# Kernel optimization log

Measured on AMD Instinct MI355X. Metric: run time of the kernel, lower is better.

Reference implementation:

```python
import jax, jax.numpy as jnp
import numpy as np
import math

B, C_LOW, C_HIGH, H, W = 8, 128, 256, 128, 128
KS = 7

def _conv(x, w, b, pad):
    out = jax.lax.conv_general_dilated(
        x, w, window_strides=(1, 1), padding=[(pad, pad), (pad, pad)],
        dimension_numbers=('NCHW', 'OIHW', 'NCHW'))
    return out + b[None, :, None, None]

def setup_inputs() -> dict:
    key = jax.random.key(0)
    ks = jax.random.split(key, 6)
    def he(k, shape):  # matches torch init: normal(0, sqrt(2/(kh*kw*out)))
        n = shape[2] * shape[3] * shape[0]
        return jax.random.normal(k, shape, jnp.float32) * math.sqrt(2.0 / n)
    return {
        'cur_low': jax.random.normal(ks[0], (B, C_LOW, H, W), jnp.float32),
        'key_low': jax.random.normal(ks[1], (B, C_LOW, H, W), jnp.float32),
        'key_high': jax.random.normal(ks[2], (B, C_HIGH, H, W), jnp.float32),
        'w_red': he(ks[3], (256, C_LOW, 3, 3)),
        'b_red': jnp.zeros((256,), jnp.float32),
        'w2': he(ks[4], (256, 512, 3, 3)),
        'b2': jnp.zeros((256,), jnp.float32),
        'w3': he(ks[5], (KS * KS, 256, 1, 1)),
        'b3': jnp.zeros((KS * KS,), jnp.float32),
    }

def reference(cur_low, key_low, key_high, w_red, b_red, w2, b2, w3, b3):
    # KernelWeightPredictor
    cur = jax.nn.relu(_conv(cur_low, w_red, b_red, 1))
    key = jax.nn.relu(_conv(key_low, w_red, b_red, 1))
    x = jax.nn.relu(_conv(jnp.concatenate([cur, key], axis=1), w2, b2, 1))
    x = jax.nn.relu(_conv(x, w3, b3, 0))            # [B, k*k, H, W]
    x = jax.nn.softmax(x, axis=1)
    b, k2, h, w = x.shape
    kernels = jnp.transpose(x, (0, 2, 3, 1)).reshape(b, h, w, KS, KS)
    # SpatiallyVariantConvolution: per-pixel 7x7 kernel applied to key_high
    pad = KS // 2
    fp = jnp.pad(key_high, ((0, 0), (0, 0), (pad, pad), (pad, pad)))
    out = jnp.zeros_like(key_high)
    for i in range(KS):          # fixed 49-iteration unrolled loop; avoids
        for j in range(KS):      # materializing the [B,C,H,W,K,K] patch tensor
            out = out + fp[:, :, i:i + h, j:j + w] * kernels[:, None, :, :, i, j]
    return out
```

## Files before the change

### kernel.cpp

```cpp
#include <hip/hip_runtime.h>
#include <stdint.h>
#include <stddef.h>

#define BN   8
#define HN   128
#define WN   128
#define HP   130
#define CLOW 128
#define CMID 256
#define KO   49

#define KHB_H 134
#define KHB_W 144
#define KHB_PLANE (KHB_H * KHB_W)

typedef __attribute__((ext_vector_type(4))) float f32x4;
typedef __attribute__((ext_vector_type(8))) short bf16x8;

typedef __attribute__((address_space(1))) const uint8_t ga_u8;
typedef __attribute__((address_space(3))) uint8_t lds_u8;

__device__ __forceinline__ short f2bf(float f) {
    uint32_t u = __float_as_uint(f);
    u += 0x7fffu + ((u >> 16) & 1u);
    return (short)(u >> 16);
}
__device__ __forceinline__ float bf2f(short s) {
    return __uint_as_float(((uint32_t)(uint16_t)s) << 16);
}
__device__ __forceinline__ void gload16(const void* g, void* l) {
    __builtin_amdgcn_global_load_lds((ga_u8*)g, (lds_u8*)l, 16, 0, 0);
}

__global__ __launch_bounds__(256) void zero_border_all_kernel(
    short* __restrict__ b0, short* __restrict__ b1,
    short* __restrict__ b2, short* __restrict__ b3) {
    const int which = blockIdx.y;
    short* buf = (which == 0) ? b0 : (which == 1) ? b1 : (which == 2) ? b2 : b3;
    const int gsh = (which < 2) ? 4 : 5;
    const int C = (which < 2) ? 128 : 256;
    int t = blockIdx.x * 256 + threadIdx.x;
    int cell = t >> gsh, g = t & ((1 << gsh) - 1);
    if (cell >= 8 * 516) return;
    int b = cell / 516, r = cell - b * 516;
    int y, x;
    if (r < 260) { y = (r >= 130) ? 129 : 0; x = (r >= 130) ? (r - 130) : r; }
    else { int j = r - 260; y = 1 + (j >> 1); x = (j & 1) ? 129 : 0; }
    uint4 z = {0u, 0u, 0u, 0u};
    *(uint4*)&buf[(((size_t)b * HP + y) * HP + x) * C + g * 8] = z;
}

__global__ __launch_bounds__(256) void convert_pad_kernel(
    const float* __restrict__ src0, const float* __restrict__ src1,
    short* __restrict__ dst0, short* __restrict__ dst1) {
    __shared__ short t[128 * 136];
    const int tid = threadIdx.x;
    const int by = blockIdx.x;
    const int b = by >> 7, y = by & 127;
    const float* src = blockIdx.y ? src1 : src0;
    short* dst = blockIdx.y ? dst1 : dst0;
    #pragma unroll
    for (int k = 0; k < 16; ++k) {
        int slot = k * 256 + tid;
        int c = slot >> 5, xg = slot & 31;
        f32x4 v = *(const f32x4*)&src[(((size_t)b * CLOW + c) * HN + y) * WN + xg * 4];
        #pragma unroll
        for (int j = 0; j < 4; ++j) t[(xg * 4 + j) * 136 + c] = f2bf(v[j]);
    }
    __syncthreads();
    short* drow = dst + (((size_t)b * HP + (y + 1)) * HP + 1) * CLOW;
    #pragma unroll
    for (int k = 0; k < 8; ++k) {
        int slot = k * 256 + tid;
        int x = slot >> 4, cg = slot & 15;
        *(bf16x8*)&drow[x * CLOW + cg * 8] = *(const bf16x8*)&t[x * 136 + cg * 8];
    }
}

__global__ __launch_bounds__(256) void pack_w_all_kernel(
    const float* __restrict__ w1, short* __restrict__ wp1,
    const float* __restrict__ w2, short* __restrict__ wp2,
    const float* __restrict__ w3, short* __restrict__ wp3) {
    int i = blockIdx.x * 256 + threadIdx.x;
    if (i < 256 * 1152 + 256 * 4608) {
        const float* w; short* wp; int CIN, K;
        if (i < 256 * 1152) { w = w1; wp = wp1; CIN = 128; K = 1152; }
        else { i -= 256 * 1152; w = w2; wp = wp2; CIN = 512; K = 4608; }
        int cout = i / K;
        int r = i - cout * K;
        int t = r >> 6;
        int j = r & 63;
        int cb = t / 9;
        int tap = t - cb * 9;
        int cin = cb * 64 + j;
        wp[i] = f2bf(w[((size_t)cout * CIN + cin) * 9 + tap]);
    } else {
        int j = i - (256 * 1152 + 256 * 4608);
        if (j >= 64 * 256) return;
        int o = j >> 8, ch = j & 255;
        wp3[j] = (o < KO) ? f2bf(w3[o * 256 + ch]) : (short)0;
    }
}

template <int CIN, bool OPAD, bool FUSE>
__global__ __launch_bounds__(512, 2) void conv_8ph_kernel(
    const short* __restrict__ in_a, const short* __restrict__ in_b,
    const short* __restrict__ wp, const float* __restrict__ bias,
    short* __restrict__ out_a, short* __restrict__ out_b,
    const short* __restrict__ w3p, const float* __restrict__ b3,
    float* __restrict__ z) {
    constexpr int K = 9 * CIN;
    constexpr int NT = K / 64;
    constexpr bool DUAL = (CIN == 512);
    constexpr int PST = DUAL ? 256 : CIN;
    extern __shared__ __align__(16) short lds[];
    const int tid = threadIdx.x;
    int bx = blockIdx.x;
    bx = (bx & 7) * 64 + (bx >> 3);
    const int b = bx >> 6, y0 = (bx & 63) << 1;
    const short* inA = DUAL ? in_a : (blockIdx.z ? in_b : in_a);
    const short* inB = DUAL ? in_b : inA;
    short* out = (!DUAL && blockIdx.z) ? out_b : out_a;

    const int lane = tid & 63, wv = tid >> 6;
    const int wm = wv >> 2, wn = wv & 3;
    const int lr = lane & 15, lk = lane >> 4;

    const int rA = tid >> 3, cc = tid & 7;
    const int cs = cc ^ (rA & 7);
    const int pthrA0 = rA * PST + cs * 8;
    const int pthrA1 = (rA + 64) * PST + cs * 8;
    const int pthrB0 = rA * K + cs * 8;
    const int pthrB1 = (rA + 64) * K + cs * 8;
    const int dA0 = rA * 64 + cc * 8;
    const int dB0 = rA * 64 + cc * 8;

    const int arow = (wm * 128 + lr) * 64;
    const int brow = (wn * 64 + lr) * 64;
    const int cof0 = ((lk) ^ (lr & 7)) * 8;
    const int cof1 = ((4 + lk) ^ (lr & 7)) * 8;

    f32x4 acc[8][4];
    f32x4 zero = {0.f, 0.f, 0.f, 0.f};
    #pragma unroll
    for (int i = 0; i < 8; ++i)
        #pragma unroll
        for (int j = 0; j < 4; ++j) acc[i][j] = zero;

    auto STAGE2 = [&](int t2, int which, short* bufA, short* bufB) {
        const int cb = (t2 * 57) >> 9;
        const int tap = t2 - cb * 9;
        const int ch0v = cb << 6;
        const short* src = (!DUAL || ch0v < 256) ? inA : inB;
        const int ch0 = DUAL ? (ch0v & 255) : ch0v;
        const int ky = (tap * 11) >> 5;
        const int kx = tap - ky * 3;
        if (which == 0 || which == 2) {
            const int po = (which == 0) ? pthrA0 : pthrA1;
            const int doff = (which == 0) ? 0 : 64 * 64;
            const short* s0 = src + ((size_t)(b * HP + (y0 + ky)) * HP + kx) * PST + ch0;
            gload16(s0 + po, bufA + doff + dA0);
            gload16(s0 + (HP * PST) + po, bufA + 128 * 64 + doff + dA0);
        } else {
            const int h2 = (which == 1) ? 0 : 1;
            const short* sb = wp + (size_t)(h2 * 128) * K + t2 * 64;
            short* d = bufB + h2 * 128 * 64 + dB0;
            gload16(sb + pthrB0, d);
            gload16(sb + pthrB1, d + 64 * 64);
        }
    };

    auto LDA = [&](const short* bufA, int mh, bf16x8 (&a)[4][2]) {
        #pragma unroll
        for (int i = 0; i < 4; ++i) {
            const int ro = arow + (mh * 64 + i * 16) * 64;
            a[i][0] = *(const bf16x8*)(bufA + ro + cof0);
            a[i][1] = *(const bf16x8*)(bufA + ro + cof1);
        }
    };
    auto LDB = [&](const short* bufB, int nh, bf16x8 (&bb)[2][2]) {
        #pragma unroll
        for (int j = 0; j < 2; ++j) {
            const int ro = brow + (nh * 32 + j * 16) * 64;
            bb[j][0] = *(const bf16x8*)(bufB + ro + cof0);
            bb[j][1] = *(const bf16x8*)(bufB + ro + cof1);
        }
    };

#define MFMA_Q(A_, B_, MH, NH) do { \
    _Pragma("unroll") \
    for (int i_ = 0; i_ < 4; ++i_) { \
        _Pragma("unroll") \
        for (int j_ = 0; j_ < 2; ++j_) { \
            acc[(MH)*4+i_][(NH)*2+j_] = __builtin_amdgcn_mfma_f32_16x16x32_bf16( \
                A_[i_][0], B_[j_][0], acc[(MH)*4+i_][(NH)*2+j_], 0, 0, 0); \
            acc[(MH)*4+i_][(NH)*2+j_] = __builtin_amdgcn_mfma_f32_16x16x32_bf16( \
                A_[i_][1], B_[j_][1], acc[(MH)*4+i_][(NH)*2+j_], 0, 0, 0); \
        } \
    } } while (0)

    short* const A0 = lds;
    short* const A1 = lds + 16384;
    short* const B0 = lds + 32768;
    short* const B1 = lds + 49152;

    STAGE2(0, 0, A0, B0); STAGE2(0, 1, A0, B0);
    STAGE2(0, 2, A0, B0); STAGE2(0, 3, A0, B0);

    auto TILE = [&](int t, short* bufA, short* bufB, short* nA, short* nB) {
        __builtin_amdgcn_s_barrier();
        __builtin_amdgcn_sched_barrier(0);
        const int t1 = t + 1;
        if (t1 < NT) {
            STAGE2(t1, 0, nA, nB); STAGE2(t1, 1, nA, nB);
            STAGE2(t1, 2, nA, nB); STAGE2(t1, 3, nA, nB);
            __builtin_amdgcn_sched_barrier(0);
            asm volatile("s_waitcnt vmcnt(8)" ::: "memory");
        } else {
            __builtin_amdgcn_sched_barrier(0);
            asm volatile("s_waitcnt vmcnt(0)" ::: "memory");
        }
        __builtin_amdgcn_sched_barrier(0);
        __builtin_amdgcn_s_barrier();
        __builtin_amdgcn_sched_barrier(0);
        bf16x8 ar[4][2], br0[2][2], br1[2][2];
        LDA(bufA, 0, ar);
        LDB(bufB, 0, br0);
        LDB(bufB, 1, br1);
        __builtin_amdgcn_s_setprio(1);
        MFMA_Q(ar, br0, 0, 0);
        MFMA_Q(ar, br1, 0, 1);
        __builtin_amdgcn_s_setprio(0);
        LDA(bufA, 1, ar);
        __builtin_amdgcn_s_setprio(1);
        MFMA_Q(ar, br0, 1, 0);
        MFMA_Q(ar, br1, 1, 1);
        __builtin_amdgcn_s_setprio(0);
    };

    for (int t = 0; t < NT; t += 2) {
        TILE(t,     A0, B0, A1, B1);
        TILE(t + 1, A1, B1, A0, B0);
    }
#undef MFMA_Q

    float bvs[4];
    #pragma unroll
    for (int nf = 0; nf < 4; ++nf) bvs[nf] = bias[wn * 64 + nf * 16 + lr];

    if constexpr (!FUSE) {
        #pragma unroll
        for (int mf = 0; mf < 8; ++mf) {
            #pragma unroll
            for (int rr = 0; rr < 4; ++rr) {
                const int p = wm * 128 + mf * 16 + lk * 4 + rr;
                const int y = y0 + (p >> 7), x = p & 127;
                short* op;
                if (OPAD)
                    op = out + ((size_t)(b * HP + (y + 1)) * HP + (x + 1)) * CMID + wn * 64 + lr;
                else
                    op = out + ((size_t)((b * HN + y) * WN + x)) * CMID + wn * 64 + lr;
                #pragma unroll
                for (int nf = 0; nf < 4; ++nf)
                    op[nf * 16] = f2bf(fmaxf(acc[mf][nf][rr] + bvs[nf], 0.f));
            }
        }
    } else {
        __syncthreads();
        short* const Xh  = lds;
        short* const W3s = lds + 32768;

        #pragma unroll
        for (int sweep = 0; sweep < 4; ++sweep) {
            const int s = sweep * 512 + tid;
            const int o = s >> 5, c = s & 31;
            gload16(w3p + o * 256 + ((c ^ (o & 7)) << 3), W3s + s * 8);
        }

        const int oo = wn * 16 + lr;
        const float b3v = (oo < KO) ? b3[oo] : 0.f;

        #pragma unroll 1
        for (int r = 0; r < 2; ++r) {
            if (wm == r) {
                #pragma unroll
                for (int nf = 0; nf < 4; ++nf) {
                    const int ch = wn * 64 + nf * 16 + lr;
                    const int ck = ch >> 3, el = ch & 7;
                    #pragma unroll
                    for (int mf = 0; mf < 8; ++mf) {
                        #pragma unroll
                        for (int rr = 0; rr < 4; ++rr) {
                            const int px = mf * 16 + lk * 4 + rr;
                            Xh[px * 256 + ((ck ^ (px & 7)) << 3) + el] =
                                f2bf(fmaxf(acc[mf][nf][rr] + bvs[nf], 0.f));
                        }
                    }
                }
            }
            __syncthreads();
            f32x4 a2[4];
            #pragma unroll
            for (int m = 0; m < 4; ++m) {
                a2[m][0] = b3v; a2[m][1] = b3v; a2[m][2] = b3v; a2[m][3] = b3v;
            }
            #pragma unroll
            for (int ks = 0; ks < 8; ++ks) {
                const bf16x8 bfr =
                    *(const bf16x8*)&W3s[oo * 256 + (((ks * 4 + lk) ^ (oo & 7)) << 3)];
                #pragma unroll
                for (int m = 0; m < 4; ++m) {
                    const int px = wm * 64 + m * 16 + lr;
                    const bf16x8 afr =
                        *(const bf16x8*)&Xh[px * 256 + (((ks * 4 + lk) ^ (px & 7)) << 3)];
                    a2[m] = __builtin_amdgcn_mfma_f32_16x16x32_bf16(afr, bfr, a2[m], 0, 0, 0);
                }
            }
            float* zp = z + ((size_t)(b * 16384 + (y0 + r) * 128)) * 64;
            #pragma unroll
            for (int m = 0; m < 4; ++m) {
                #pragma unroll
                for (int r2 = 0; r2 < 4; ++r2) {
                    const int px = wm * 64 + m * 16 + lk * 4 + r2;
                    zp[px * 64 + oo] = a2[m][r2];
                }
            }
            if (r == 0) __syncthreads();
        }
    }
}

__global__ __launch_bounds__(256) void pad_kh_kernel(
    const float* __restrict__ kh, short* __restrict__ khb) {
    const int bc = blockIdx.x;
    const float* src = kh + (size_t)bc * (HN * WN);
    short* dst = khb + (size_t)bc * KHB_PLANE;
    for (int i = threadIdx.x; i < KHB_H * (KHB_W / 8); i += 256) {
        int yy = i / (KHB_W / 8);
        int g = i - yy * (KHB_W / 8);
        int ys = yy - 3;
        bf16x8 v;
        #pragma unroll
        for (int t = 0; t < 8; ++t) {
            int xs = g * 8 + t - 4;
            float f = 0.f;
            if ((unsigned)ys < 128u && (unsigned)xs < 128u) f = src[(ys << 7) + xs];
            v[t] = f2bf(f);
        }
        *(bf16x8*)&dst[yy * KHB_W + g * 8] = v;
    }
}

__global__ __launch_bounds__(256) void svc4_kernel(
    const float* __restrict__ z, const short* __restrict__ khb,
    float* __restrict__ out) {
    __shared__ float a_s[KO * 64];
    const int tid = threadIdx.x;
    int by = blockIdx.y;
    by = (by & 7) * 128 + (by >> 3);
    const int b = by >> 7, y = by & 127;
    const int x0 = blockIdx.x * 64;

    {
        const int px = tid >> 2, l = tid & 3;
        const float* zp = z + ((size_t)(b * 16384 + (y << 7) + x0 + px)) * 64 + l * 16;
        float v[16];
        #pragma unroll
        for (int q = 0; q < 4; ++q) {
            f32x4 t4 = *(const f32x4*)&zp[q * 4];
            v[q * 4 + 0] = fmaxf(t4[0], 0.f);
            v[q * 4 + 1] = fmaxf(t4[1], 0.f);
            v[q * 4 + 2] = fmaxf(t4[2], 0.f);
            v[q * 4 + 3] = fmaxf(t4[3], 0.f);
        }
        #pragma unroll
        for (int j = 1; j < 16; ++j) if (l == 3) v[j] = -1e30f;
        float m = v[0];
        #pragma unroll
        for (int j = 1; j < 16; ++j) m = fmaxf(m, v[j]);
        m = fmaxf(m, __shfl_xor(m, 1, 64));
        m = fmaxf(m, __shfl_xor(m, 2, 64));
        float s = 0.f;
        #pragma unroll
        for (int j = 0; j < 16; ++j) { v[j] = __expf(v[j] - m); s += v[j]; }
        s += __shfl_xor(s, 1, 64);
        s += __shfl_xor(s, 2, 64);
        const float inv = 1.f / s;
        #pragma unroll
        for (int j = 0; j < 16; ++j) {
            const int o = l * 16 + j;
            if (o < KO) a_s[o * 64 + px] = v[j] * inv;
        }
    }
    __syncthreads();

    const int ci = tid >> 3;
    const int pg = tid & 7;
    const int p0 = x0 + pg * 8;

    float acc[8][8];
    #pragma unroll
    for (int c = 0; c < 8; ++c)
        #pragma unroll
        for (int j = 0; j < 8; ++j) acc[c][j] = 0.f;

    const short* kbase = khb + (((size_t)b * 256 + ci) * KHB_H + y) * KHB_W + p0;

    #pragma unroll 1
    for (int dy = 0; dy < 7; ++dy) {
        f32x4 av[14];
        #pragma unroll
        for (int dx = 0; dx < 7; ++dx) {
            av[dx * 2]     = *(const f32x4*)&a_s[(dy * 7 + dx) * 64 + pg * 8];
            av[dx * 2 + 1] = *(const f32x4*)&a_s[(dy * 7 + dx) * 64 + pg * 8 + 4];
        }
        const short* krow = kbase + dy * KHB_W;
        #pragma unroll
        for (int c = 0; c < 8; ++c) {
            const short* kp = krow + (size_t)c * 32 * KHB_PLANE;
            bf16x8 k0 = *(const bf16x8*)(kp);
            bf16x8 k1 = *(const bf16x8*)(kp + 8);
            float win[16];
            #pragma unroll
            for (int t = 0; t < 8; ++t) { win[t] = bf2f(k0[t]); win[t + 8] = bf2f(k1[t]); }
            #pragma unroll
            for (int dx = 0; dx < 7; ++dx) {
                #pragma unroll
                for (int j = 0; j < 8; ++j)
                    acc[c][j] = fmaf(win[j + dx + 1], av[dx * 2 + (j >> 2)][j & 3],
                                     acc[c][j]);
            }
        }
    }

    #pragma unroll
    for (int c = 0; c < 8; ++c) {
        float* op = out + (((size_t)b * 256 + ci + c * 32) << 14) + (y << 7) + p0;
        f32x4 r0 = {acc[c][0], acc[c][1], acc[c][2], acc[c][3]};
        f32x4 r1 = {acc[c][4], acc[c][5], acc[c][6], acc[c][7]};
        *(f32x4*)op = r0;
        *(f32x4*)(op + 4) = r1;
    }
}

extern "C" void kernel_launch(void* const* d_in, const int* in_sizes, int n_in,
                              void* d_out, int out_size, void* d_ws, size_t ws_size,
                              hipStream_t stream) {
    (void)in_sizes; (void)n_in; (void)out_size; (void)ws_size;
    const float* cur_low  = (const float*)d_in[0];
    const float* key_low  = (const float*)d_in[1];
    const float* key_high = (const float*)d_in[2];
    const float* w_red    = (const float*)d_in[3];
    const float* b_red    = (const float*)d_in[4];
    const float* w2       = (const float*)d_in[5];
    const float* b2       = (const float*)d_in[6];
    const float* w3       = (const float*)d_in[7];
    const float* b3       = (const float*)d_in[8];
    float* out = (float*)d_out;
    char* ws = (char*)d_ws;

    const size_t SZ_XPAD = (size_t)BN * HP * HP * CLOW * 2;
    const size_t SZ_YPAD = (size_t)BN * HP * HP * CMID * 2;
    short* xpadc = (short*)(ws);
    short* xpadk = (short*)(ws + SZ_XPAD);
    short* ypadc = (short*)(ws + 2 * SZ_XPAD);
    short* ypadk = (short*)(ws + 2 * SZ_XPAD + SZ_YPAD);
    short* w1p   = (short*)(ws + 2 * SZ_XPAD + 2 * SZ_YPAD);
    short* w2p   = w1p + (size_t)256 * 1152;
    float* z     = (float*)(ws);
    short* khb   = (short*)(ws + 2 * SZ_XPAD);
    short* w3p   = (short*)((char*)d_out + (size_t)134217728 - 32768);

    hipFuncSetAttribute((const void*)conv_8ph_kernel<128, true, false>,
                        hipFuncAttributeMaxDynamicSharedMemorySize, 131072);
    hipFuncSetAttribute((const void*)conv_8ph_kernel<512, false, true>,
                        hipFuncAttributeMaxDynamicSharedMemorySize, 131072);

    zero_border_all_kernel<<<dim3(516, 4), 256, 0, stream>>>(xpadc, xpadk, ypadc, ypadk);
    convert_pad_kernel<<<dim3(1024, 2), 256, 0, stream>>>(cur_low, key_low, xpadc, xpadk);
    pack_w_all_kernel<<<(256 * (1152 + 4608) + 64 * 256 + 255) / 256, 256, 0, stream>>>(
        w_red, w1p, w2, w2p, w3, w3p);

    conv_8ph_kernel<128, true, false><<<dim3(512, 1, 2), 512, 131072, stream>>>(
        xpadc, xpadk, w1p, b_red, ypadc, ypadk, nullptr, nullptr, nullptr);

    conv_8ph_kernel<512, false, true><<<dim3(512, 1, 1), 512, 131072, stream>>>(
        ypadc, ypadk, w2p, b2, nullptr, nullptr, w3p, b3, z);

    pad_kh_kernel<<<2048, 256, 0, stream>>>(key_high, khb);
    svc4_kernel<<<dim3(2, 1024), 256, 0, stream>>>(z, khb, out);
}
```

Baseline: 661.8 us.

## Load conv weight fragments directly from global into registers, halve LDS

The implicit-GEMM conv kernels no longer stage the weight (B) tiles through LDS. Each lane now loads its MFMA B fragments straight from global memory into registers every K-step, and only the activation tiles stay double-buffered in LDS. This cuts LDS traffic and the LDS footprint (dynamic shared memory drops to 64KB or 96KB), which may let more blocks share a CU. In exchange, the global weight loads sit on the critical path with no prefetch, and pad_kh is separately vectorised to use float4 loads.

New measurement: 971.0 us. +46.7%, slower.

```diff
diff --git a/kernel.cpp b/kernel.cpp
--- a/kernel.cpp
+++ b/kernel.cpp
@@ -130,16 +130,17 @@
     const int cs = cc ^ (rA & 7);
     const int pthrA0 = rA * PST + cs * 8;
     const int pthrA1 = (rA + 64) * PST + cs * 8;
-    const int pthrB0 = rA * K + cs * 8;
-    const int pthrB1 = (rA + 64) * K + cs * 8;
     const int dA0 = rA * 64 + cc * 8;
-    const int dB0 = rA * 64 + cc * 8;
 
     const int arow = (wm * 128 + lr) * 64;
-    const int brow = (wn * 64 + lr) * 64;
     const int cof0 = ((lk) ^ (lr & 7)) * 8;
     const int cof1 = ((4 + lk) ^ (lr & 7)) * 8;
 
+    const short* wB[4];
+    #pragma unroll
+    for (int nf = 0; nf < 4; ++nf)
+        wB[nf] = wp + (size_t)(wn * 64 + nf * 16 + lr) * K + (lk << 3);
+
     f32x4 acc[8][4];
     f32x4 zero = {0.f, 0.f, 0.f, 0.f};
     #pragma unroll
@@ -147,7 +148,7 @@
         #pragma unroll
         for (int j = 0; j < 4; ++j) acc[i][j] = zero;
 
-    auto STAGE2 = [&](int t2, int which, short* bufA, short* bufB) {
+    auto STAGE_A = [&](int t2, short* bufA) {
         const int cb = (t2 * 57) >> 9;
         const int tap = t2 - cb * 9;
         const int ch0v = cb << 6;
@@ -155,19 +156,11 @@
         const int ch0 = DUAL ? (ch0v & 255) : ch0v;
         const int ky = (tap * 11) >> 5;
         const int kx = tap - ky * 3;
-        if (which == 0 || which == 2) {
-            const int po = (which == 0) ? pthrA0 : pthrA1;
-            const int doff = (which == 0) ? 0 : 64 * 64;
-            const short* s0 = src + ((size_t)(b * HP + (y0 + ky)) * HP + kx) * PST + ch0;
-            gload16(s0 + po, bufA + doff + dA0);
-            gload16(s0 + (HP * PST) + po, bufA + 128 * 64 + doff + dA0);
-        } else {
-            const int h2 = (which == 1) ? 0 : 1;
-            const short* sb = wp + (size_t)(h2 * 128) * K + t2 * 64;
-            short* d = bufB + h2 * 128 * 64 + dB0;
-            gload16(sb + pthrB0, d);
-            gload16(sb + pthrB1, d + 64 * 64);
-        }
+        const short* s0 = src + ((size_t)(b * HP + (y0 + ky)) * HP + kx) * PST + ch0;
+        gload16(s0 + pthrA0, bufA + dA0);
+        gload16(s0 + (HP * PST) + pthrA0, bufA + 128 * 64 + dA0);
+        gload16(s0 + pthrA1, bufA + 64 * 64 + dA0);
+        gload16(s0 + (HP * PST) + pthrA1, bufA + 192 * 64 + dA0);
     };
 
     auto LDA = [&](const short* bufA, int mh, bf16x8 (&a)[4][2]) {
@@ -176,14 +169,6 @@
             const int ro = arow + (mh * 64 + i * 16) * 64;
             a[i][0] = *(const bf16x8*)(bufA + ro + cof0);
             a[i][1] = *(const bf16x8*)(bufA + ro + cof1);
-        }
-    };
-    auto LDB = [&](const short* bufB, int nh, bf16x8 (&bb)[2][2]) {
-        #pragma unroll
-        for (int j = 0; j < 2; ++j) {
-            const int ro = brow + (nh * 32 + j * 16) * 64;
-            bb[j][0] = *(const bf16x8*)(bufB + ro + cof0);
-            bb[j][1] = *(const bf16x8*)(bufB + ro + cof1);
         }
     };
 
@@ -193,29 +178,32 @@
         _Pragma("unroll") \
         for (int j_ = 0; j_ < 2; ++j_) { \
             acc[(MH)*4+i_][(NH)*2+j_] = __builtin_amdgcn_mfma_f32_16x16x32_bf16( \
-                A_[i_][0], B_[j_][0], acc[(MH)*4+i_][(NH)*2+j_], 0, 0, 0); \
+                A_[i_][0], B_[(NH)*2+j_][0], acc[(MH)*4+i_][(NH)*2+j_], 0, 0, 0); \
             acc[(MH)*4+i_][(NH)*2+j_] = __builtin_amdgcn_mfma_f32_16x16x32_bf16( \
-                A_[i_][1], B_[j_][1], acc[(MH)*4+i_][(NH)*2+j_], 0, 0, 0); \
+                A_[i_][1], B_[(NH)*2+j_][1], acc[(MH)*4+i_][(NH)*2+j_], 0, 0, 0); \
         } \
     } } while (0)
 
     short* const A0 = lds;
     short* const A1 = lds + 16384;
-    short* const B0 = lds + 32768;
-    short* const B1 = lds + 49152;
-
-    STAGE2(0, 0, A0, B0); STAGE2(0, 1, A0, B0);
-    STAGE2(0, 2, A0, B0); STAGE2(0, 3, A0, B0);
-
-    auto TILE = [&](int t, short* bufA, short* bufB, short* nA, short* nB) {
+
+    STAGE_A(0, A0);
+
+    auto TILE = [&](int t, short* bufA, short* nA) {
         __builtin_amdgcn_s_barrier();
+        __builtin_amdgcn_sched_barrier(0);
+        bf16x8 bf[4][2];
+        #pragma unroll
+        for (int nf = 0; nf < 4; ++nf) {
+            bf[nf][0] = *(const bf16x8*)(wB[nf] + t * 64);
+            bf[nf][1] = *(const bf16x8*)(wB[nf] + t * 64 + 32);
+        }
         __builtin_amdgcn_sched_barrier(0);
         const int t1 = t + 1;
         if (t1 < NT) {
-            STAGE2(t1, 0, nA, nB); STAGE2(t1, 1, nA, nB);
-            STAGE2(t1, 2, nA, nB); STAGE2(t1, 3, nA, nB);
+            STAGE_A(t1, nA);
             __builtin_amdgcn_sched_barrier(0);
-            asm volatile("s_waitcnt vmcnt(8)" ::: "memory");
+            asm volatile("s_waitcnt vmcnt(4)" ::: "memory");
         } else {
             __builtin_amdgcn_sched_barrier(0);
             asm volatile("s_waitcnt vmcnt(0)" ::: "memory");
@@ -223,24 +211,22 @@
         __builtin_amdgcn_sched_barrier(0);
         __builtin_amdgcn_s_barrier();
         __builtin_amdgcn_sched_barrier(0);
-        bf16x8 ar[4][2], br0[2][2], br1[2][2];
+        bf16x8 ar[4][2];
         LDA(bufA, 0, ar);
-        LDB(bufB, 0, br0);
-        LDB(bufB, 1, br1);
         __builtin_amdgcn_s_setprio(1);
-        MFMA_Q(ar, br0, 0, 0);
-        MFMA_Q(ar, br1, 0, 1);
+        MFMA_Q(ar, bf, 0, 0);
+        MFMA_Q(ar, bf, 0, 1);
         __builtin_amdgcn_s_setprio(0);
         LDA(bufA, 1, ar);
         __builtin_amdgcn_s_setprio(1);
-        MFMA_Q(ar, br0, 1, 0);
-        MFMA_Q(ar, br1, 1, 1);
+        MFMA_Q(ar, bf, 1, 0);
+        MFMA_Q(ar, bf, 1, 1);
         __builtin_amdgcn_s_setprio(0);
     };
 
     for (int t = 0; t < NT; t += 2) {
-        TILE(t,     A0, B0, A1, B1);
-        TILE(t + 1, A1, B1, A0, B0);
+        TILE(t,     A0, A1);
+        TILE(t + 1, A1, A0);
     }
 #undef MFMA_Q
 
@@ -335,18 +321,20 @@
     const int bc = blockIdx.x;
     const float* src = kh + (size_t)bc * (HN * WN);
     short* dst = khb + (size_t)bc * KHB_PLANE;
-    for (int i = threadIdx.x; i < KHB_H * (KHB_W / 8); i += 256) {
-        int yy = i / (KHB_W / 8);
-        int g = i - yy * (KHB_W / 8);
-        int ys = yy - 3;
+    for (int u = threadIdx.x; u < KHB_H * 18; u += 256) {
+        const int yy = (u * 3641) >> 16;
+        const int g = u - yy * 18;
+        const int ys = yy - 3;
+        const int xb = g * 8 - 4;
+        f32x4 lo = {0.f, 0.f, 0.f, 0.f}, hi = {0.f, 0.f, 0.f, 0.f};
+        if ((unsigned)ys < 128u) {
+            const float* row = src + (ys << 7);
+            if ((unsigned)xb < 125u)       lo = *(const f32x4*)(row + xb);
+            if ((unsigned)(xb + 4) < 125u) hi = *(const f32x4*)(row + xb + 4);
+        }
         bf16x8 v;
         #pragma unroll
-        for (int t = 0; t < 8; ++t) {
-            int xs = g * 8 + t - 4;
-            float f = 0.f;
-            if ((unsigned)ys < 128u && (unsigned)xs < 128u) f = src[(ys << 7) + xs];
-            v[t] = f2bf(f);
-        }
+        for (int t = 0; t < 4; ++t) { v[t] = f2bf(lo[t]); v[t + 4] = f2bf(hi[t]); }
         *(bf16x8*)&dst[yy * KHB_W + g * 8] = v;
     }
 }
@@ -472,19 +460,19 @@
     short* w3p   = (short*)((char*)d_out + (size_t)134217728 - 32768);
 
     hipFuncSetAttribute((const void*)conv_8ph_kernel<128, true, false>,
-                        hipFuncAttributeMaxDynamicSharedMemorySize, 131072);
+                        hipFuncAttributeMaxDynamicSharedMemorySize, 65536);
     hipFuncSetAttribute((const void*)conv_8ph_kernel<512, false, true>,
-                        hipFuncAttributeMaxDynamicSharedMemorySize, 131072);
+                        hipFuncAttributeMaxDynamicSharedMemorySize, 98304);
 
     zero_border_all_kernel<<<dim3(516, 4), 256, 0, stream>>>(xpadc, xpadk, ypadc, ypadk);
     convert_pad_kernel<<<dim3(1024, 2), 256, 0, stream>>>(cur_low, key_low, xpadc, xpadk);
     pack_w_all_kernel<<<(256 * (1152 + 4608) + 64 * 256 + 255) / 256, 256, 0, stream>>>(
         w_red, w1p, w2, w2p, w3, w3p);
 
-    conv_8ph_kernel<128, true, false><<<dim3(512, 1, 2), 512, 131072, stream>>>(
+    conv_8ph_kernel<128, true, false><<<dim3(512, 1, 2), 512, 65536, stream>>>(
         xpadc, xpadk, w1p, b_red, ypadc, ypadk, nullptr, nullptr, nullptr);
 
-    conv_8ph_kernel<512, false, true><<<dim3(512, 1, 1), 512, 131072, stream>>>(
+    conv_8ph_kernel<512, false, true><<<dim3(512, 1, 1), 512, 98304, stream>>>(
         ypadc, ypadk, w2p, b2, nullptr, nullptr, w3p, b3, z);
 
     pad_kh_kernel<<<2048, 256, 0, stream>>>(key_high, khb);
```
